# Kernel tuning notes

Hardware: AMD Instinct MI355X
Metric: run time of the kernel (lower is better)

Reference implementation:

```python
import jax, jax.numpy as jnp
import numpy as np

N_NODES = 100000
N_EDGES = 1600000
IN_DIM = 64
HID_DIM = 128
OUT_DIM = 128


def setup_inputs() -> dict:
    key = jax.random.key(0)
    ks = jax.random.split(key, 12)
    s = 0.05
    return {
        "x": jax.random.normal(ks[0], (N_NODES, IN_DIM), jnp.float32),
        "edge_index": jax.random.randint(ks[1], (2, N_EDGES), 0, N_NODES, jnp.int64),
        "edge_attr": jax.random.uniform(ks[2], (N_EDGES, 2), jnp.float32),
        # conv1 MLP: Linear(IN+2, HID) -> ReLU -> Linear(HID, HID)
        "W11": jax.random.normal(ks[3], (IN_DIM + 2, HID_DIM), jnp.float32) * s,
        "b11": jax.random.normal(ks[4], (HID_DIM,), jnp.float32) * s,
        "W12": jax.random.normal(ks[5], (HID_DIM, HID_DIM), jnp.float32) * s,
        "b12": jax.random.normal(ks[6], (HID_DIM,), jnp.float32) * s,
        # conv2 MLP: Linear(HID+2, OUT) -> ReLU -> Linear(OUT, OUT)
        "W21": jax.random.normal(ks[7], (HID_DIM + 2, OUT_DIM), jnp.float32) * s,
        "b21": jax.random.normal(ks[8], (OUT_DIM,), jnp.float32) * s,
        "W22": jax.random.normal(ks[9], (OUT_DIM, OUT_DIM), jnp.float32) * s,
        "b22": jax.random.normal(ks[10], (OUT_DIM,), jnp.float32) * s,
    }


def _gin_conv(x, edge_index, edge_attr, W1, b1, W2, b2):
    N = x.shape[0]
    loop = jnp.arange(N, dtype=edge_index.dtype)
    src = jnp.concatenate([edge_index[0], loop])  # [E+N] message sources
    dst = jnp.concatenate([edge_index[1], loop])  # [E+N] aggregation targets
    # self-loop edge_attr filled with 1.0 (PyG add_self_loops default)
    ea = jnp.concatenate([edge_attr, jnp.ones((N, edge_attr.shape[1]), edge_attr.dtype)], axis=0)
    m = jnp.concatenate([x[src], ea], axis=-1)  # [E+N, F+2] gather + concat
    h = jnp.dot(jax.nn.relu(jnp.dot(m, W1) + b1), W2) + b2  # edge MLP
    return jax.ops.segment_sum(h, dst, num_segments=N)  # scatter-add aggregate


def reference(x, edge_index, edge_attr, W11, b11, W12, b12, W21, b21, W22, b22):
    h = _gin_conv(x, edge_index, edge_attr, W11, b11, W12, b12)
    h = jax.nn.relu(h)
    return _gin_conv(h, edge_index, edge_attr, W21, b21, W22, b22)
```

## Files before the change

### kernel.cpp

```cpp
#include <hip/hip_runtime.h>


typedef unsigned int uint;
typedef __attribute__((ext_vector_type(8))) short bf16x8;
typedef __attribute__((ext_vector_type(4))) float f32x4;

#define BSHIFT 10
#define BNODES (1 << BSHIFT)

static __device__ __forceinline__ unsigned short f2bf(float f) {
    uint u = __float_as_uint(f);
    uint r = (u + 0x7fffu + ((u >> 16) & 1u)) >> 16;
    return (unsigned short)r;
}


__global__ void wprep_all(const float* __restrict__ W11, const float* __restrict__ W12,
                          const float* __restrict__ W21, const float* __restrict__ W22,
                          unsigned short* Wt11, unsigned short* Wt12,
                          unsigned short* Wt21, unsigned short* Wt22,
                          int* bcnt, int* ptr, int N, int E) {
    int idx = blockIdx.x * 256 + threadIdx.x;
    if (idx < 128) bcnt[idx] = 0;
    if (idx == 128) ptr[N] = E;
    const float* W; unsigned short* Wt; int K; int off;
    if (idx < 64 * 128)        { W = W11; Wt = Wt11; K = 64;  off = idx; }
    else if (idx < 192 * 128)  { W = W12; Wt = Wt12; K = 128; off = idx - 64 * 128; }
    else if (idx < 320 * 128)  { W = W21; Wt = Wt21; K = 128; off = idx - 192 * 128; }
    else if (idx < 448 * 128)  { W = W22; Wt = Wt22; K = 128; off = idx - 320 * 128; }
    else return;
    int k = off >> 7, n = off & 127;
    Wt[n * K + k] = f2bf(W[k * 128 + n]);
}


__global__ __launch_bounds__(512) void bin_kernel(
    const int* __restrict__ src, const int* __restrict__ dst,
    const float* __restrict__ ea, int* __restrict__ bcnt,
    int2* __restrict__ barr, int CAP, int E, int B) {
    __shared__ int hist[128];
    __shared__ int bbase[128];
    __shared__ int gbase[128];
    __shared__ int2 sorted[4096];
    __shared__ unsigned char bof[4096];
    const int tileBase = blockIdx.x * 4096;
    int n = E - tileBase; if (n > 4096) n = 4096; if (n <= 0) return;
    const int tid = threadIdx.x;
    if (tid < 128) hist[tid] = 0;
    __syncthreads();

    int2 ent[8]; int bk[8]; int rk[8];
#pragma unroll
    for (int k = 0; k < 8; k++) {
        int i = k * 512 + tid;
        bk[k] = -1;
        if (i < n) {
            int e = tileBase + i;
            int s = src[e], d = dst[e];
            float2 a = reinterpret_cast<const float2*>(ea)[e];
            int b = d >> BSHIFT;
            int dloc = d & (BNODES - 1);
            ent[k].x = s | (dloc << 17);
            ent[k].y = (int)((uint)f2bf(a.x) | ((uint)f2bf(a.y) << 16));
            bk[k] = b;
            rk[k] = atomicAdd(&hist[b], 1);
        }
    }
    __syncthreads();
    if (tid == 0) {
        int run = 0;
        for (int b = 0; b < B; b++) { bbase[b] = run; run += hist[b]; }
    }
    __syncthreads();
    if (tid < B && hist[tid] > 0) gbase[tid] = atomicAdd(&bcnt[tid], hist[tid]);
    __syncthreads();
#pragma unroll
    for (int k = 0; k < 8; k++) {
        if (bk[k] >= 0) {
            int p = bbase[bk[k]] + rk[k];
            sorted[p] = ent[k];
            bof[p] = (unsigned char)bk[k];
        }
    }
    __syncthreads();
    for (int i = tid; i < n; i += 512) {
        int b = bof[i];
        barr[(long)b * CAP + gbase[b] + (i - bbase[b])] = sorted[i];
    }
}


__global__ __launch_bounds__(1024) void bucket_csr(
    const int2* __restrict__ barr, const int* __restrict__ bcnt,
    int CAP, int N, int B,
    int2* __restrict__ csr, int* __restrict__ ptr) {
    __shared__ int hist[BNODES];
    __shared__ int scn[BNODES];
    __shared__ int lptr[BNODES];
    const int g = blockIdx.x;
    const int tid = threadIdx.x;
    const int cnt = bcnt[g];
    int base = 0;
    for (int b = 0; b < g; b++) base += bcnt[b];

    hist[tid] = 0;
    __syncthreads();
    const int2* my = barr + (long)g * CAP;
    for (int i = tid; i < cnt; i += 1024) {
        int dloc = ((uint)my[i].x) >> 17;
        atomicAdd(&hist[dloc], 1);
    }
    __syncthreads();
    int v = hist[tid];
    scn[tid] = v;
    __syncthreads();
    for (int off = 1; off < 1024; off <<= 1) {
        int t = (tid >= off) ? scn[tid - off] : 0;
        __syncthreads();
        scn[tid] += t;
        __syncthreads();
    }
    int excl = scn[tid] - v;
    lptr[tid] = excl;
    long gnode = (long)g * BNODES + tid;
    if (gnode < (long)N) ptr[gnode] = base + excl;
    __syncthreads();
    for (int i = tid; i < cnt; i += 1024) {
        int2 e = my[i];
        int dloc = ((uint)e.x) >> 17;
        int pos = base + atomicAdd(&lptr[dloc], 1);
        int2 o; o.x = e.x & 0x1FFFF; o.y = e.y;
        csr[pos] = o;
    }
}


__global__ __launch_bounds__(256) void gather_kernel(
    const uint* __restrict__ Au, const int* __restrict__ ptr,
    const int2* __restrict__ csr, const float* __restrict__ we,
    uint* __restrict__ B, int N) {
    int node = blockIdx.x * 4 + (threadIdx.x >> 6);
    if (node >= N) return;
    int t = threadIdx.x & 63;
    int c = 2 * t;
    float w0x = we[c], w0y = we[c + 1];
    float w1x = we[128 + c], w1y = we[128 + c + 1];

    const char* Ab = (const char*)Au;
    const uint t4 = (uint)t * 4u;
#define LD(sidx) (*(const uint*)(Ab + ((((uint)(sidx)) << 8) + t4)))
#define ACC(rv, ev)                                                      \
    {                                                                    \
        float a0 = __uint_as_float(((uint)(ev)) << 16);                  \
        float a1 = __uint_as_float(((uint)(ev)) & 0xffff0000u);          \
        float vx = __uint_as_float((rv) << 16);                          \
        float vy = __uint_as_float((rv) & 0xffff0000u);                  \
        vx = fmaf(a0, w0x, fmaf(a1, w1x, vx));                           \
        vy = fmaf(a0, w0y, fmaf(a1, w1y, vy));                           \
        ax += fmaxf(vx, 0.f);                                            \
        ay += fmaxf(vy, 0.f);                                            \
    }
    uint selfv = LD(node);
    float ax = fmaxf(__uint_as_float(selfv << 16) + w0x + w1x, 0.f);
    float ay = fmaxf(__uint_as_float(selfv & 0xffff0000u) + w0y + w1y, 0.f);

    int k   = __builtin_amdgcn_readfirstlane(ptr[node]);
    int end = __builtin_amdgcn_readfirstlane(ptr[node + 1]);

    for (; k + 8 <= end; k += 8) {
        int2 c0 = csr[k],     c1 = csr[k + 1], c2 = csr[k + 2], c3 = csr[k + 3];
        int2 c4 = csr[k + 4], c5 = csr[k + 5], c6 = csr[k + 6], c7 = csr[k + 7];
        uint r0 = LD(c0.x); uint r1 = LD(c1.x); uint r2 = LD(c2.x); uint r3 = LD(c3.x);
        uint r4 = LD(c4.x); uint r5 = LD(c5.x); uint r6 = LD(c6.x); uint r7 = LD(c7.x);
        ACC(r0, c0.y) ACC(r1, c1.y) ACC(r2, c2.y) ACC(r3, c3.y)
        ACC(r4, c4.y) ACC(r5, c5.y) ACC(r6, c6.y) ACC(r7, c7.y)
    }
    for (; k + 2 <= end; k += 2) {
        int2 c0 = csr[k], c1 = csr[k + 1];
        uint r0 = LD(c0.x); uint r1 = LD(c1.x);
        ACC(r0, c0.y) ACC(r1, c1.y)
    }
    if (k < end) {
        int2 c0 = csr[k];
        uint r0 = LD(c0.x);
        ACC(r0, c0.y)
    }
#undef ACC
#undef LD
    B[(long)node * 64 + t] = (uint)f2bf(ax) | ((uint)f2bf(ay) << 16);
}


template <int K, bool IN_F32, bool OUT_BF16, bool USE_CNT, bool RELU>
__global__ __launch_bounds__(256) void gemm_mfma(
    const void* __restrict__ Ain, const unsigned short* __restrict__ Wt,
    const float* __restrict__ bias, const int* __restrict__ ptr,
    void* __restrict__ Cout, int N) {
    constexpr int KS = K / 32;
    const int wave = threadIdx.x >> 6;
    const int lane = threadIdx.x & 63;
    const int m = lane & 15, quad = lane >> 4;
    const long rowBase = (long)blockIdx.x * 64;

    bf16x8 bfrag[2][KS];
#pragma unroll
    for (int ct = 0; ct < 2; ct++) {
        int col = (wave * 2 + ct) * 16 + m;
#pragma unroll
        for (int ks = 0; ks < KS; ks++)
            bfrag[ct][ks] = *(const bf16x8*)(Wt + (long)col * K + ks * 32 + quad * 8);
    }

#pragma unroll
    for (int rt = 0; rt < 4; rt++) {
        long row = rowBase + rt * 16 + m;
        long rc = row < N ? row : (long)N - 1;
        bf16x8 afrag[KS];
        if (IN_F32) {
            const float* arow = (const float*)Ain + rc * K;
#pragma unroll
            for (int ks = 0; ks < KS; ks++) {
                float4 lo = *(const float4*)(arow + ks * 32 + quad * 8);
                float4 hi = *(const float4*)(arow + ks * 32 + quad * 8 + 4);
                bf16x8 f;
                f[0] = (short)f2bf(lo.x); f[1] = (short)f2bf(lo.y);
                f[2] = (short)f2bf(lo.z); f[3] = (short)f2bf(lo.w);
                f[4] = (short)f2bf(hi.x); f[5] = (short)f2bf(hi.y);
                f[6] = (short)f2bf(hi.z); f[7] = (short)f2bf(hi.w);
                afrag[ks] = f;
            }
        } else {
            const unsigned short* arow = (const unsigned short*)Ain + rc * K;
#pragma unroll
            for (int ks = 0; ks < KS; ks++)
                afrag[ks] = *(const bf16x8*)(arow + ks * 32 + quad * 8);
        }

#pragma unroll
        for (int ct = 0; ct < 2; ct++) {
            f32x4 acc = {0.f, 0.f, 0.f, 0.f};
#pragma unroll
            for (int ks = 0; ks < KS; ks++)
                acc = __builtin_amdgcn_mfma_f32_16x16x32_bf16(afrag[ks], bfrag[ct][ks], acc, 0, 0, 0);

            int col = (wave * 2 + ct) * 16 + m;
            float b = bias[col];
#pragma unroll
            for (int r = 0; r < 4; r++) {
                long orow = rowBase + rt * 16 + quad * 4 + r;
                if (orow < N) {
                    float v = acc[r];
                    if (USE_CNT) v += b * (float)(ptr[orow + 1] - ptr[orow] + 1);
                    else v += b;
                    if (RELU) v = fmaxf(v, 0.f);
                    if (OUT_BF16) ((unsigned short*)Cout)[orow * 128 + col] = f2bf(v);
                    else ((float*)Cout)[orow * 128 + col] = v;
                }
            }
        }
    }
}


__global__ __launch_bounds__(256) void fused_mid_gemm(
    const unsigned short* __restrict__ Bin, const int* __restrict__ ptr,
    const unsigned short* __restrict__ WtA, const float* __restrict__ biasA,
    const unsigned short* __restrict__ WtB, const float* __restrict__ biasB,
    unsigned short* __restrict__ Cout, int N) {
    __shared__ unsigned short ts[64 * 136];
    const int wave = threadIdx.x >> 6;
    const int lane = threadIdx.x & 63;
    const int m = lane & 15, quad = lane >> 4;
    const long rowBase = (long)blockIdx.x * 64;

    bf16x8 bfrag[2][4];
#pragma unroll
    for (int ct = 0; ct < 2; ct++) {
        int col = (wave * 2 + ct) * 16 + m;
#pragma unroll
        for (int ks = 0; ks < 4; ks++)
            bfrag[ct][ks] = *(const bf16x8*)(WtA + (long)col * 128 + ks * 32 + quad * 8);
    }

    f32x4 acc[4][2];
#pragma unroll
    for (int rt = 0; rt < 4; rt++) {
        long row = rowBase + rt * 16 + m;
        long rc = row < N ? row : (long)N - 1;
        const unsigned short* arow = Bin + rc * 128;
        bf16x8 af[4];
#pragma unroll
        for (int ks = 0; ks < 4; ks++)
            af[ks] = *(const bf16x8*)(arow + ks * 32 + quad * 8);
#pragma unroll
        for (int ct = 0; ct < 2; ct++) {
            f32x4 a = {0.f, 0.f, 0.f, 0.f};
#pragma unroll
            for (int ks = 0; ks < 4; ks++)
                a = __builtin_amdgcn_mfma_f32_16x16x32_bf16(af[ks], bfrag[ct][ks], a, 0, 0, 0);
            acc[rt][ct] = a;
        }
    }

#pragma unroll
    for (int rt = 0; rt < 4; rt++) {
        float cntf[4];
#pragma unroll
        for (int r = 0; r < 4; r++) {
            long grow = rowBase + rt * 16 + quad * 4 + r;
            cntf[r] = (grow < N) ? (float)(ptr[grow + 1] - ptr[grow] + 1) : 1.f;
        }
#pragma unroll
        for (int ct = 0; ct < 2; ct++) {
            int col = (wave * 2 + ct) * 16 + m;
            float b = biasA[col];
#pragma unroll
            for (int r = 0; r < 4; r++) {
                int row = rt * 16 + quad * 4 + r;
                ts[row * 136 + col] = f2bf(fmaxf(acc[rt][ct][r] + b * cntf[r], 0.f));
            }
        }
    }
    __syncthreads();

#pragma unroll
    for (int ct = 0; ct < 2; ct++) {
        int col = (wave * 2 + ct) * 16 + m;
#pragma unroll
        for (int ks = 0; ks < 4; ks++)
            bfrag[ct][ks] = *(const bf16x8*)(WtB + (long)col * 128 + ks * 32 + quad * 8);
    }
#pragma unroll
    for (int rt = 0; rt < 4; rt++) {
        const unsigned short* lr = ts + (rt * 16 + m) * 136;
        bf16x8 af[4];
#pragma unroll
        for (int ks = 0; ks < 4; ks++)
            af[ks] = *(const bf16x8*)(lr + ks * 32 + quad * 8);
#pragma unroll
        for (int ct = 0; ct < 2; ct++) {
            f32x4 a = {0.f, 0.f, 0.f, 0.f};
#pragma unroll
            for (int ks = 0; ks < 4; ks++)
                a = __builtin_amdgcn_mfma_f32_16x16x32_bf16(af[ks], bfrag[ct][ks], a, 0, 0, 0);
            int col = (wave * 2 + ct) * 16 + m;
            float b = biasB[col];
#pragma unroll
            for (int r = 0; r < 4; r++) {
                long grow = rowBase + rt * 16 + quad * 4 + r;
                if (grow < N) Cout[grow * 128 + col] = f2bf(a[r] + b);
            }
        }
    }
}


extern "C" void kernel_launch(void* const* d_in, const int* in_sizes, int n_in,
                              void* d_out, int out_size, void* d_ws, size_t ws_size,
                              hipStream_t stream) {
    const float* x   = (const float*)d_in[0];
    const int*   ei  = (const int*)d_in[1];
    const float* ea  = (const float*)d_in[2];
    const float* W11 = (const float*)d_in[3];
    const float* b11 = (const float*)d_in[4];
    const float* W12 = (const float*)d_in[5];
    const float* b12 = (const float*)d_in[6];
    const float* W21 = (const float*)d_in[7];
    const float* b21 = (const float*)d_in[8];
    const float* W22 = (const float*)d_in[9];
    const float* b22 = (const float*)d_in[10];
    float* out = (float*)d_out;

    const int N = in_sizes[0] / 64;
    const int E = in_sizes[1] / 2;
    const int* src = ei;
    const int* dst = ei + E;

    const int B = (N + BNODES - 1) >> BSHIFT;
    const int CAP = E / B + 4096;

    char* p = (char*)d_ws;
    unsigned short* A_bf = (unsigned short*)p;  p += (size_t)N * 128 * 2;
    unsigned short* B_bf = (unsigned short*)p;
    int2* barr = (int2*)B_bf;                   p += (size_t)N * 128 * 2;
    int2* csr  = (int2*)p;                      p += (size_t)E * 8;
    int* ptr   = (int*)p;                       p += (size_t)(N + 1) * 4;
    int* bcnt  = (int*)p;                       p += 128 * 4;
    unsigned short* Wt11 = (unsigned short*)p;  p += (size_t)64 * 128 * 2;
    unsigned short* Wt12 = (unsigned short*)p;  p += (size_t)128 * 128 * 2;
    unsigned short* Wt21 = (unsigned short*)p;  p += (size_t)128 * 128 * 2;
    unsigned short* Wt22 = (unsigned short*)p;

    const int binBlocks = (E + 4095) / 4096;
    const int gatherBlocks = (N + 3) / 4;
    const int tileBlocks = (N + 63) / 64;

    wprep_all<<<(448 * 128 + 255) / 256, 256, 0, stream>>>(W11, W12, W21, W22,
                                                           Wt11, Wt12, Wt21, Wt22,
                                                           bcnt, ptr, N, E);
    bin_kernel<<<binBlocks, 512, 0, stream>>>(src, dst, ea, bcnt, barr, CAP, E, B);
    bucket_csr<<<B, 1024, 0, stream>>>(barr, bcnt, CAP, N, B, csr, ptr);

    gemm_mfma<64, true, true, false, false><<<tileBlocks, 256, 0, stream>>>(
        x, Wt11, b11, nullptr, A_bf, N);
    gather_kernel<<<gatherBlocks, 256, 0, stream>>>((const uint*)A_bf, ptr, csr,
                                                    W11 + 64 * 128, (uint*)B_bf, N);
    fused_mid_gemm<<<tileBlocks, 256, 0, stream>>>(B_bf, ptr, Wt12, b12, Wt21, b21, A_bf, N);
    gather_kernel<<<gatherBlocks, 256, 0, stream>>>((const uint*)A_bf, ptr, csr,
                                                    W21 + 128 * 128, (uint*)B_bf, N);
    gemm_mfma<128, false, false, true, false><<<tileBlocks, 256, 0, stream>>>(
        B_bf, Wt22, b22, ptr, out, N);
}
```

Before: 369.4 us.

## Fuse CSR build with first GEMM, halve bucket size, use warp-shuffle scans

Buckets shrink to 512 nodes, which gives 196 buckets instead of 98 and more CSR-build blocks. The bucket-to-CSR pass is merged into one launch with the first-layer GEMM, so the two independent jobs run concurrently in a single grid. The shared-memory prefix scans in the binning and CSR kernels become wave-shuffle scans, and the serial per-bucket base sum becomes a shared atomic reduction. The gather kernel now uses readfirstlane on the edge indices to make them scalar, a 4-wide tail loop and nontemporal output stores. This adds code complexity, and the binning kernel still stores the bucket id in an 8-bit field, which now has to hold up to 196.

```diff
diff --git a/kernel.cpp b/kernel.cpp
--- a/kernel.cpp
+++ b/kernel.cpp
@@ -5,7 +5,7 @@
 typedef __attribute__((ext_vector_type(8))) short bf16x8;
 typedef __attribute__((ext_vector_type(4))) float f32x4;
 
-#define BSHIFT 10
+#define BSHIFT 9
 #define BNODES (1 << BSHIFT)
 
 static __device__ __forceinline__ unsigned short f2bf(float f) {
@@ -21,8 +21,8 @@
                           unsigned short* Wt21, unsigned short* Wt22,
                           int* bcnt, int* ptr, int N, int E) {
     int idx = blockIdx.x * 256 + threadIdx.x;
-    if (idx < 128) bcnt[idx] = 0;
-    if (idx == 128) ptr[N] = E;
+    if (idx < 256) bcnt[idx] = 0;
+    if (idx == 0) ptr[N] = E;
     const float* W; unsigned short* Wt; int K; int off;
     if (idx < 64 * 128)        { W = W11; Wt = Wt11; K = 64;  off = idx; }
     else if (idx < 192 * 128)  { W = W12; Wt = Wt12; K = 128; off = idx - 64 * 128; }
@@ -38,48 +38,57 @@
     const int* __restrict__ src, const int* __restrict__ dst,
     const float* __restrict__ ea, int* __restrict__ bcnt,
     int2* __restrict__ barr, int CAP, int E, int B) {
-    __shared__ int hist[128];
-    __shared__ int bbase[128];
-    __shared__ int gbase[128];
+    __shared__ int hist[256];
+    __shared__ int bbase[256];
+    __shared__ int gbase[256];
+    __shared__ int wtot[4];
     __shared__ int2 sorted[4096];
     __shared__ unsigned char bof[4096];
     const int tileBase = blockIdx.x * 4096;
     int n = E - tileBase; if (n > 4096) n = 4096; if (n <= 0) return;
     const int tid = threadIdx.x;
-    if (tid < 128) hist[tid] = 0;
+    const int lane = tid & 63;
+    if (tid < 256) hist[tid] = 0;
     __syncthreads();
 
     int2 ent[8]; int bk[8]; int rk[8];
 #pragma unroll
-    for (int k = 0; k < 8; k++) {
-        int i = k * 512 + tid;
-        bk[k] = -1;
+    for (int kk = 0; kk < 8; kk++) {
+        int i = kk * 512 + tid;
+        bk[kk] = -1;
         if (i < n) {
             int e = tileBase + i;
             int s = src[e], d = dst[e];
             float2 a = reinterpret_cast<const float2*>(ea)[e];
             int b = d >> BSHIFT;
             int dloc = d & (BNODES - 1);
-            ent[k].x = s | (dloc << 17);
-            ent[k].y = (int)((uint)f2bf(a.x) | ((uint)f2bf(a.y) << 16));
-            bk[k] = b;
-            rk[k] = atomicAdd(&hist[b], 1);
-        }
-    }
-    __syncthreads();
-    if (tid == 0) {
-        int run = 0;
-        for (int b = 0; b < B; b++) { bbase[b] = run; run += hist[b]; }
-    }
-    __syncthreads();
+            ent[kk].x = s | (dloc << 17);
+            ent[kk].y = (int)((uint)f2bf(a.x) | ((uint)f2bf(a.y) << 16));
+            bk[kk] = b;
+            rk[kk] = atomicAdd(&hist[b], 1);
+        }
+    }
+    __syncthreads();
+    int hv = (tid < 256) ? hist[tid] : 0;
+    int inc = hv;
+#pragma unroll
+    for (int off = 1; off < 64; off <<= 1) {
+        int tt = __shfl_up(inc, off, 64);
+        if (lane >= off) inc += tt;
+    }
+    if ((tid >> 6) < 4 && lane == 63) wtot[tid >> 6] = inc;
+    __syncthreads();
+    if (tid == 0) { int run = 0; for (int i = 0; i < 4; i++) { int tt = wtot[i]; wtot[i] = run; run += tt; } }
+    __syncthreads();
+    if (tid < 256) bbase[tid] = inc - hv + wtot[tid >> 6];
     if (tid < B && hist[tid] > 0) gbase[tid] = atomicAdd(&bcnt[tid], hist[tid]);
     __syncthreads();
 #pragma unroll
-    for (int k = 0; k < 8; k++) {
-        if (bk[k] >= 0) {
-            int p = bbase[bk[k]] + rk[k];
-            sorted[p] = ent[k];
-            bof[p] = (unsigned char)bk[k];
+    for (int kk = 0; kk < 8; kk++) {
+        if (bk[kk] >= 0) {
+            int p = bbase[bk[kk]] + rk[kk];
+            sorted[p] = ent[kk];
+            bof[p] = (unsigned char)bk[kk];
         }
     }
     __syncthreads();
@@ -90,47 +99,142 @@
 }
 
 
-__global__ __launch_bounds__(1024) void bucket_csr(
-    const int2* __restrict__ barr, const int* __restrict__ bcnt,
-    int CAP, int N, int B,
-    int2* __restrict__ csr, int* __restrict__ ptr) {
+static __device__ void csr_body(const int2* __restrict__ barr, const int* __restrict__ bcnt,
+                                int CAP, int N, int2* __restrict__ csr, int* __restrict__ ptr) {
     __shared__ int hist[BNODES];
-    __shared__ int scn[BNODES];
     __shared__ int lptr[BNODES];
+    __shared__ int wtot[8];
+    __shared__ int sbase;
     const int g = blockIdx.x;
     const int tid = threadIdx.x;
+    const int lane = tid & 63;
     const int cnt = bcnt[g];
-    int base = 0;
-    for (int b = 0; b < g; b++) base += bcnt[b];
-
+    if (tid == 0) sbase = 0;
     hist[tid] = 0;
     __syncthreads();
+    if (tid < g) atomicAdd(&sbase, bcnt[tid]);
     const int2* my = barr + (long)g * CAP;
-    for (int i = tid; i < cnt; i += 1024) {
-        int dloc = ((uint)my[i].x) >> 17;
-        atomicAdd(&hist[dloc], 1);
-    }
+    for (int i = tid; i < cnt; i += 512)
+        atomicAdd(&hist[((uint)my[i].x) >> 17], 1);
     __syncthreads();
     int v = hist[tid];
-    scn[tid] = v;
-    __syncthreads();
-    for (int off = 1; off < 1024; off <<= 1) {
-        int t = (tid >= off) ? scn[tid - off] : 0;
-        __syncthreads();
-        scn[tid] += t;
-        __syncthreads();
-    }
-    int excl = scn[tid] - v;
+    int inc = v;
+#pragma unroll
+    for (int off = 1; off < 64; off <<= 1) {
+        int tt = __shfl_up(inc, off, 64);
+        if (lane >= off) inc += tt;
+    }
+    if (lane == 63) wtot[tid >> 6] = inc;
+    __syncthreads();
+    if (tid == 0) { int run = 0; for (int i = 0; i < 8; i++) { int tt = wtot[i]; wtot[i] = run; run += tt; } }
+    __syncthreads();
+    const int base = sbase;
+    int excl = inc - v + wtot[tid >> 6];
     lptr[tid] = excl;
-    long gnode = (long)g * BNODES + tid;
-    if (gnode < (long)N) ptr[gnode] = base + excl;
-    __syncthreads();
-    for (int i = tid; i < cnt; i += 1024) {
+    int gnode = g * BNODES + tid;
+    if (gnode < N) ptr[gnode] = base + excl;
+    __syncthreads();
+    for (int i = tid; i < cnt; i += 512) {
         int2 e = my[i];
-        int dloc = ((uint)e.x) >> 17;
-        int pos = base + atomicAdd(&lptr[dloc], 1);
+        int pos = base + atomicAdd(&lptr[((uint)e.x) >> 17], 1);
         int2 o; o.x = e.x & 0x1FFFF; o.y = e.y;
         csr[pos] = o;
+    }
+}
+
+
+template <int K, bool IN_F32, bool OUT_BF16, bool USE_CNT, bool RELU>
+static __device__ __forceinline__ void gemm_body(
+    const void* __restrict__ Ain, const unsigned short* __restrict__ Wt,
+    const float* __restrict__ bias, const int* __restrict__ ptr,
+    void* __restrict__ Cout, int N, int tid, long rowBase) {
+    constexpr int KS = K / 32;
+    const int wave = tid >> 6;
+    const int lane = tid & 63;
+    const int m = lane & 15, quad = lane >> 4;
+
+    bf16x8 bfrag[2][KS];
+#pragma unroll
+    for (int ct = 0; ct < 2; ct++) {
+        int col = (wave * 2 + ct) * 16 + m;
+#pragma unroll
+        for (int ks = 0; ks < KS; ks++)
+            bfrag[ct][ks] = *(const bf16x8*)(Wt + (long)col * K + ks * 32 + quad * 8);
+    }
+
+#pragma unroll
+    for (int rt = 0; rt < 4; rt++) {
+        long row = rowBase + rt * 16 + m;
+        long rc = row < N ? row : (long)N - 1;
+        bf16x8 afrag[KS];
+        if (IN_F32) {
+            const float* arow = (const float*)Ain + rc * K;
+#pragma unroll
+            for (int ks = 0; ks < KS; ks++) {
+                float4 lo = *(const float4*)(arow + ks * 32 + quad * 8);
+                float4 hi = *(const float4*)(arow + ks * 32 + quad * 8 + 4);
+                bf16x8 f;
+                f[0] = (short)f2bf(lo.x); f[1] = (short)f2bf(lo.y);
+                f[2] = (short)f2bf(lo.z); f[3] = (short)f2bf(lo.w);
+                f[4] = (short)f2bf(hi.x); f[5] = (short)f2bf(hi.y);
+                f[6] = (short)f2bf(hi.z); f[7] = (short)f2bf(hi.w);
+                afrag[ks] = f;
+            }
+        } else {
+            const unsigned short* arow = (const unsigned short*)Ain + rc * K;
+#pragma unroll
+            for (int ks = 0; ks < KS; ks++)
+                afrag[ks] = *(const bf16x8*)(arow + ks * 32 + quad * 8);
+        }
+
+#pragma unroll
+        for (int ct = 0; ct < 2; ct++) {
+            f32x4 acc = {0.f, 0.f, 0.f, 0.f};
+#pragma unroll
+            for (int ks = 0; ks < KS; ks++)
+                acc = __builtin_amdgcn_mfma_f32_16x16x32_bf16(afrag[ks], bfrag[ct][ks], acc, 0, 0, 0);
+
+            int col = (wave * 2 + ct) * 16 + m;
+            float b = bias[col];
+#pragma unroll
+            for (int r = 0; r < 4; r++) {
+                long orow = rowBase + rt * 16 + quad * 4 + r;
+                if (orow < N) {
+                    float v = acc[r];
+                    if (USE_CNT) v += b * (float)(ptr[orow + 1] - ptr[orow] + 1);
+                    else v += b;
+                    if (RELU) v = fmaxf(v, 0.f);
+                    if (OUT_BF16) ((unsigned short*)Cout)[orow * 128 + col] = f2bf(v);
+                    else ((float*)Cout)[orow * 128 + col] = v;
+                }
+            }
+        }
+    }
+}
+
+template <int K, bool IN_F32, bool OUT_BF16, bool USE_CNT, bool RELU>
+__global__ __launch_bounds__(256) void gemm_mfma(
+    const void* __restrict__ Ain, const unsigned short* __restrict__ Wt,
+    const float* __restrict__ bias, const int* __restrict__ ptr,
+    void* __restrict__ Cout, int N) {
+    gemm_body<K, IN_F32, OUT_BF16, USE_CNT, RELU>(Ain, Wt, bias, ptr, Cout, N,
+                                                  threadIdx.x, (long)blockIdx.x * 64);
+}
+
+
+__global__ __launch_bounds__(512) void csr_gemm1(
+    const int2* __restrict__ barr, const int* __restrict__ bcnt, int CAP, int N,
+    int2* __restrict__ csr, int* __restrict__ ptr, int CSRB,
+    const float* __restrict__ x, const unsigned short* __restrict__ Wt11,
+    const float* __restrict__ b11, unsigned short* __restrict__ A_bf) {
+    if ((int)blockIdx.x < CSRB) {
+        csr_body(barr, bcnt, CAP, N, csr, ptr);
+    } else {
+        int bid = blockIdx.x - CSRB;
+        int sub = threadIdx.x >> 8;
+        gemm_body<64, true, true, false, false>(x, Wt11, b11, nullptr, A_bf, N,
+                                                threadIdx.x & 255,
+                                                (long)bid * 128 + sub * 64);
     }
 }
 
@@ -138,13 +242,14 @@
 __global__ __launch_bounds__(256) void gather_kernel(
     const uint* __restrict__ Au, const int* __restrict__ ptr,
     const int2* __restrict__ csr, const float* __restrict__ we,
-    uint* __restrict__ B, int N) {
+    uint* __restrict__ Bout, int N) {
     int node = blockIdx.x * 4 + (threadIdx.x >> 6);
     if (node >= N) return;
-    int t = threadIdx.x & 63;
-    int c = 2 * t;
-    float w0x = we[c], w0y = we[c + 1];
-    float w1x = we[128 + c], w1y = we[128 + c + 1];
+    node = __builtin_amdgcn_readfirstlane(node);
+    const int t = threadIdx.x & 63;
+    const int c = 2 * t;
+    const float w0x = we[c], w0y = we[c + 1];
+    const float w1x = we[128 + c], w1y = we[128 + c + 1];
 
     const char* Ab = (const char*)Au;
     const uint t4 = (uint)t * 4u;
@@ -160,7 +265,12 @@
         ax += fmaxf(vx, 0.f);                                            \
         ay += fmaxf(vy, 0.f);                                            \
     }
-    uint selfv = LD(node);
+#define EDGE(i, off)                                                     \
+    int2 c##i = csr[k + (off)];                                          \
+    uint s##i = (uint)__builtin_amdgcn_readfirstlane(c##i.x);            \
+    uint e##i = (uint)__builtin_amdgcn_readfirstlane(c##i.y);
+
+    uint selfv = LD((uint)node);
     float ax = fmaxf(__uint_as_float(selfv << 16) + w0x + w1x, 0.f);
     float ay = fmaxf(__uint_as_float(selfv & 0xffff0000u) + w0y + w1y, 0.f);
 
@@ -168,97 +278,28 @@
     int end = __builtin_amdgcn_readfirstlane(ptr[node + 1]);
 
     for (; k + 8 <= end; k += 8) {
-        int2 c0 = csr[k],     c1 = csr[k + 1], c2 = csr[k + 2], c3 = csr[k + 3];
-        int2 c4 = csr[k + 4], c5 = csr[k + 5], c6 = csr[k + 6], c7 = csr[k + 7];
-        uint r0 = LD(c0.x); uint r1 = LD(c1.x); uint r2 = LD(c2.x); uint r3 = LD(c3.x);
-        uint r4 = LD(c4.x); uint r5 = LD(c5.x); uint r6 = LD(c6.x); uint r7 = LD(c7.x);
-        ACC(r0, c0.y) ACC(r1, c1.y) ACC(r2, c2.y) ACC(r3, c3.y)
-        ACC(r4, c4.y) ACC(r5, c5.y) ACC(r6, c6.y) ACC(r7, c7.y)
-    }
-    for (; k + 2 <= end; k += 2) {
-        int2 c0 = csr[k], c1 = csr[k + 1];
-        uint r0 = LD(c0.x); uint r1 = LD(c1.x);
-        ACC(r0, c0.y) ACC(r1, c1.y)
-    }
-    if (k < end) {
-        int2 c0 = csr[k];
-        uint r0 = LD(c0.x);
-        ACC(r0, c0.y)
-    }
+        EDGE(0, 0) EDGE(1, 1) EDGE(2, 2) EDGE(3, 3)
+        EDGE(4, 4) EDGE(5, 5) EDGE(6, 6) EDGE(7, 7)
+        uint r0 = LD(s0); uint r1 = LD(s1); uint r2 = LD(s2); uint r3 = LD(s3);
+        uint r4 = LD(s4); uint r5 = LD(s5); uint r6 = LD(s6); uint r7 = LD(s7);
+        ACC(r0, e0) ACC(r1, e1) ACC(r2, e2) ACC(r3, e3)
+        ACC(r4, e4) ACC(r5, e5) ACC(r6, e6) ACC(r7, e7)
+    }
+    for (; k + 4 <= end; k += 4) {
+        EDGE(0, 0) EDGE(1, 1) EDGE(2, 2) EDGE(3, 3)
+        uint r0 = LD(s0); uint r1 = LD(s1); uint r2 = LD(s2); uint r3 = LD(s3);
+        ACC(r0, e0) ACC(r1, e1) ACC(r2, e2) ACC(r3, e3)
+    }
+    for (; k < end; k++) {
+        EDGE(0, 0)
+        uint r0 = LD(s0);
+        ACC(r0, e0)
+    }
+#undef EDGE
 #undef ACC
 #undef LD
-    B[(long)node * 64 + t] = (uint)f2bf(ax) | ((uint)f2bf(ay) << 16);
-}
-
-
-template <int K, bool IN_F32, bool OUT_BF16, bool USE_CNT, bool RELU>
-__global__ __launch_bounds__(256) void gemm_mfma(
-    const void* __restrict__ Ain, const unsigned short* __restrict__ Wt,
-    const float* __restrict__ bias, const int* __restrict__ ptr,
-    void* __restrict__ Cout, int N) {
-    constexpr int KS = K / 32;
-    const int wave = threadIdx.x >> 6;
-    const int lane = threadIdx.x & 63;
-    const int m = lane & 15, quad = lane >> 4;
-    const long rowBase = (long)blockIdx.x * 64;
-
-    bf16x8 bfrag[2][KS];
-#pragma unroll
-    for (int ct = 0; ct < 2; ct++) {
-        int col = (wave * 2 + ct) * 16 + m;
-#pragma unroll
-        for (int ks = 0; ks < KS; ks++)
-            bfrag[ct][ks] = *(const bf16x8*)(Wt + (long)col * K + ks * 32 + quad * 8);
-    }
-
-#pragma unroll
-    for (int rt = 0; rt < 4; rt++) {
-        long row = rowBase + rt * 16 + m;
-        long rc = row < N ? row : (long)N - 1;
-        bf16x8 afrag[KS];
-        if (IN_F32) {
-            const float* arow = (const float*)Ain + rc * K;
-#pragma unroll
-            for (int ks = 0; ks < KS; ks++) {
-                float4 lo = *(const float4*)(arow + ks * 32 + quad * 8);
-                float4 hi = *(const float4*)(arow + ks * 32 + quad * 8 + 4);
-                bf16x8 f;
-                f[0] = (short)f2bf(lo.x); f[1] = (short)f2bf(lo.y);
-                f[2] = (short)f2bf(lo.z); f[3] = (short)f2bf(lo.w);
-                f[4] = (short)f2bf(hi.x); f[5] = (short)f2bf(hi.y);
-                f[6] = (short)f2bf(hi.z); f[7] = (short)f2bf(hi.w);
-                afrag[ks] = f;
-            }
-        } else {
-            const unsigned short* arow = (const unsigned short*)Ain + rc * K;
-#pragma unroll
-            for (int ks = 0; ks < KS; ks++)
-                afrag[ks] = *(const bf16x8*)(arow + ks * 32 + quad * 8);
-        }
-
-#pragma unroll
-        for (int ct = 0; ct < 2; ct++) {
-            f32x4 acc = {0.f, 0.f, 0.f, 0.f};
-#pragma unroll
-            for (int ks = 0; ks < KS; ks++)
-                acc = __builtin_amdgcn_mfma_f32_16x16x32_bf16(afrag[ks], bfrag[ct][ks], acc, 0, 0, 0);
-
-            int col = (wave * 2 + ct) * 16 + m;
-            float b = bias[col];
-#pragma unroll
-            for (int r = 0; r < 4; r++) {
-                long orow = rowBase + rt * 16 + quad * 4 + r;
-                if (orow < N) {
-                    float v = acc[r];
-                    if (USE_CNT) v += b * (float)(ptr[orow + 1] - ptr[orow] + 1);
-                    else v += b;
-                    if (RELU) v = fmaxf(v, 0.f);
-                    if (OUT_BF16) ((unsigned short*)Cout)[orow * 128 + col] = f2bf(v);
-                    else ((float*)Cout)[orow * 128 + col] = v;
-                }
-            }
-        }
-    }
+    uint outv = (uint)f2bf(ax) | ((uint)f2bf(ay) << 16);
+    __builtin_nontemporal_store(outv, Bout + (long)node * 64 + t);
 }
 
 
@@ -385,7 +426,7 @@
     int2* barr = (int2*)B_bf;                   p += (size_t)N * 128 * 2;
     int2* csr  = (int2*)p;                      p += (size_t)E * 8;
     int* ptr   = (int*)p;                       p += (size_t)(N + 1) * 4;
-    int* bcnt  = (int*)p;                       p += 128 * 4;
+    int* bcnt  = (int*)p;                       p += 256 * 4;
     unsigned short* Wt11 = (unsigned short*)p;  p += (size_t)64 * 128 * 2;
     unsigned short* Wt12 = (unsigned short*)p;  p += (size_t)128 * 128 * 2;
     unsigned short* Wt21 = (unsigned short*)p;  p += (size_t)128 * 128 * 2;
@@ -394,15 +435,14 @@
     const int binBlocks = (E + 4095) / 4096;
     const int gatherBlocks = (N + 3) / 4;
     const int tileBlocks = (N + 63) / 64;
-
-    wprep_all<<<(448 * 128 + 255) / 256, 256, 0, stream>>>(W11, W12, W21, W22,
-                                                           Wt11, Wt12, Wt21, Wt22,
-                                                           bcnt, ptr, N, E);
+    const int g1Tiles = (N + 127) / 128;
+
+    wprep_all<<<224, 256, 0, stream>>>(W11, W12, W21, W22,
+                                       Wt11, Wt12, Wt21, Wt22,
+                                       bcnt, ptr, N, E);
     bin_kernel<<<binBlocks, 512, 0, stream>>>(src, dst, ea, bcnt, barr, CAP, E, B);
-    bucket_csr<<<B, 1024, 0, stream>>>(barr, bcnt, CAP, N, B, csr, ptr);
-
-    gemm_mfma<64, true, true, false, false><<<tileBlocks, 256, 0, stream>>>(
-        x, Wt11, b11, nullptr, A_bf, N);
+    csr_gemm1<<<B + g1Tiles, 512, 0, stream>>>(barr, bcnt, CAP, N, csr, ptr, B,
+                                               x, Wt11, b11, A_bf);
     gather_kernel<<<gatherBlocks, 256, 0, stream>>>((const uint*)A_bf, ptr, csr,
                                                     W11 + 64 * 128, (uint*)B_bf, N);
     fused_mid_gemm<<<tileBlocks, 256, 0, stream>>>(B_bf, ptr, Wt12, b12, Wt21, b21, A_bf, N);
```

Result: no change. 364.0 us (-1.5%).
